# Optimization experiments

Hardware: AMD Instinct MI355X
Metric: run time of the kernel (lower is better)

## Reference

```python
import jax, jax.numpy as jnp
import numpy as np

NUM_EMBEDDINGS = 1024
EMBEDDING_DIM = 256
BETA = 0.25


def setup_inputs() -> dict:
    key = jax.random.key(0)
    k1, k2 = jax.random.split(key)
    inputs = jax.random.normal(k1, (32, EMBEDDING_DIM, 64, 64), dtype=jnp.float32)
    # codebook init: uniform(-1/K, 1/K), matching nn.Embedding init in the module
    embedding = jax.random.uniform(
        k2, (NUM_EMBEDDINGS, EMBEDDING_DIM), dtype=jnp.float32,
        minval=-1.0 / NUM_EMBEDDINGS, maxval=1.0 / NUM_EMBEDDINGS)
    return {"inputs": inputs, "embedding": embedding, "beta": BETA}


def reference(inputs, embedding, beta):
    # inputs: [B, D, H, W] -> [B, H, W, D]
    x = jnp.transpose(inputs, (0, 2, 3, 1))
    in_shape = x.shape
    flat = x.reshape(-1, embedding.shape[1])  # [N, D]
    dist = (jnp.sum(flat * flat, axis=1, keepdims=True)
            + jnp.sum(embedding * embedding, axis=1)
            - 2.0 * flat @ embedding.T)
    codebook_indices = jnp.argmin(dist, axis=1)  # [N]
    quantized = embedding[codebook_indices].reshape(in_shape)  # [B,H,W,D]
    sg = jax.lax.stop_gradient
    e_latent_loss = beta * jnp.mean((sg(quantized) - x) ** 2)
    q_latent_loss = jnp.mean((quantized - sg(x)) ** 2)
    loss = e_latent_loss + q_latent_loss
    # straight-through estimator
    quantized_st = x + sg(quantized - x)
    return loss, jnp.transpose(quantized_st, (0, 3, 1, 2))
```

## Files before the change

kernel.cpp:

```cpp
#include <hip/hip_runtime.h>
#include <hip/hip_bf16.h>


#define DIN 256
#define NCODES 1024

typedef __attribute__((ext_vector_type(8))) short short8;
typedef __attribute__((ext_vector_type(4))) float float4v;
typedef __attribute__((ext_vector_type(2))) float float2v;
typedef __attribute__((ext_vector_type(4))) unsigned short ushort4v;

static __device__ __forceinline__ unsigned short f2bf(float f) {
  unsigned int u = __float_as_uint(f);
  unsigned int r = (u + 0x7fffu + ((u >> 16) & 1u)) >> 16;
  return (unsigned short)r;
}

__global__ void vq_prep(const float* __restrict__ e,
                        unsigned short* __restrict__ e_bf2,
                        float* __restrict__ norms) {
  int wave = threadIdx.x >> 6, lane = threadIdx.x & 63;
  int k = blockIdx.x * 4 + wave;
  float4v v = ((const float4v*)(e + k * DIN))[lane];
  float ss = v[0]*v[0] + v[1]*v[1] + v[2]*v[2] + v[3]*v[3];
  ushort4v pk;
  pk[0] = f2bf(v[0]); pk[1] = f2bf(v[1]); pk[2] = f2bf(v[2]); pk[3] = f2bf(v[3]);
  int cc = lane >> 1, sub = lane & 1;
  *(ushort4v*)(e_bf2 + (cc * NCODES + k) * 8 + sub * 4) = pk;
  #pragma unroll
  for (int m = 1; m < 64; m <<= 1) ss += __shfl_xor(ss, m, 64);
  if (lane == 0) norms[k] = ss;
}

__global__ void __launch_bounds__(256, 4)
vq_main(const float* __restrict__ xin, const float* __restrict__ e_fp,
        const unsigned short* __restrict__ e_bf2, const float* __restrict__ norms,
        float* __restrict__ out, float* __restrict__ loss_acc) {
  __shared__ char smem[34080];
  unsigned short* es = (unsigned short*)smem;
  float* qs  = (float*)smem;
  float* vs  = (float*)(smem + 32768);
  int*   is_ = (int*)  (smem + 33280);
  int*   fi  = (int*)  (smem + 33792);
  float* rs  = (float*)(smem + 34048);

  const int tid  = threadIdx.x;
  const int wave = tid >> 6, lane = tid & 63;
  const int m16  = lane & 15, quad = lane >> 4;
  const int wr   = wave >> 1, wc = wave & 1;
  const int b    = blockIdx.x >> 6, h = blockIdx.x & 63;
  const int base = b * 1048576 + h * 64;

  short8 areg[16];
  #pragma unroll
  for (int i = 0; i < 2; ++i) {
    int r = wr * 32 + i * 16 + m16;
    #pragma unroll
    for (int kk = 0; kk < 8; ++kk) {
      int cc = kk * 4 + quad;
      short8 pk;
      #pragma unroll
      for (int ii = 0; ii < 8; ++ii)
        pk[ii] = (short)f2bf(xin[base + (cc * 8 + ii) * 4096 + r]);
      areg[i * 8 + kk] = pk;
    }
  }

  float bestv[2][4];
  int   besti[2][4];
  float4v acc[2][2];
  #pragma unroll
  for (int i = 0; i < 2; ++i) {
    #pragma unroll
    for (int r = 0; r < 4; ++r) { bestv[i][r] = INFINITY; besti[i][r] = 0; }
    #pragma unroll
    for (int j = 0; j < 2; ++j) acc[i][j] = (float4v)(0.0f);
  }

  for (int ct = 0; ct < 16; ++ct) {
    int c0 = ct * 64;
    #pragma unroll
    for (int q = 0; q < 8; ++q) {
      int cc8 = wave * 8 + q;
      const unsigned short* gsrc = e_bf2 + (cc8 * NCODES + c0) * 8 + lane * 8;
      unsigned short* ldst = es + cc8 * 512;
      __builtin_amdgcn_global_load_lds(
          (const __attribute__((address_space(1))) void*)gsrc,
          (__attribute__((address_space(3))) void*)ldst, 16, 0, 0);
    }
    __syncthreads();
    #pragma unroll
    for (int kk = 0; kk < 8; ++kk) {
      int cc = kk * 4 + quad;
      short8 b0 = *(short8*)(es + (cc * 64 + wc * 32 + m16) * 8);
      short8 b1 = *(short8*)(es + (cc * 64 + wc * 32 + 16 + m16) * 8);
      acc[0][0] = __builtin_amdgcn_mfma_f32_16x16x32_bf16(areg[kk],     b0, acc[0][0], 0, 0, 0);
      acc[0][1] = __builtin_amdgcn_mfma_f32_16x16x32_bf16(areg[kk],     b1, acc[0][1], 0, 0, 0);
      acc[1][0] = __builtin_amdgcn_mfma_f32_16x16x32_bf16(areg[8 + kk], b0, acc[1][0], 0, 0, 0);
      acc[1][1] = __builtin_amdgcn_mfma_f32_16x16x32_bf16(areg[8 + kk], b1, acc[1][1], 0, 0, 0);
    }
    #pragma unroll
    for (int j = 0; j < 2; ++j) {
      int col = c0 + wc * 32 + j * 16 + m16;
      float nj = norms[col];
      #pragma unroll
      for (int i = 0; i < 2; ++i) {
        #pragma unroll
        for (int r = 0; r < 4; ++r) {
          float s = nj - 2.0f * acc[i][j][r];
          if (s < bestv[i][r]) { bestv[i][r] = s; besti[i][r] = col; }
        }
        acc[i][j] = (float4v)(0.0f);
      }
    }
    __syncthreads();
  }

  #pragma unroll
  for (int msk = 1; msk <= 8; msk <<= 1) {
    #pragma unroll
    for (int i = 0; i < 2; ++i)
      #pragma unroll
      for (int r = 0; r < 4; ++r) {
        float ov = __shfl_xor(bestv[i][r], msk, 64);
        int   oi = __shfl_xor(besti[i][r], msk, 64);
        if (ov < bestv[i][r] || (ov == bestv[i][r] && oi < besti[i][r])) {
          bestv[i][r] = ov; besti[i][r] = oi;
        }
      }
  }
  if (m16 == 0) {
    #pragma unroll
    for (int i = 0; i < 2; ++i)
      #pragma unroll
      for (int r = 0; r < 4; ++r) {
        int rl = wr * 32 + i * 16 + quad * 4 + r;
        vs [rl * 2 + wc] = bestv[i][r];
        is_[rl * 2 + wc] = besti[i][r];
      }
  }
  __syncthreads();
  if (tid < 64) {
    float v0 = vs[tid * 2], v1 = vs[tid * 2 + 1];
    int   i0 = is_[tid * 2], i1 = is_[tid * 2 + 1];
    fi[tid] = (v1 < v0 || (v1 == v0 && i1 < i0)) ? i1 : i0;
  }
  __syncthreads();

  float lsum = 0.0f;
  const int wq = tid & 31, dL0 = tid >> 5;
  for (int h2 = 0; h2 < 4; ++h2) {
    #pragma unroll
    for (int j = 0; j < 4; ++j) {
      int f = j * 256 + tid;
      int w2 = f >> 4, cc = f & 15;
      int idx = fi[w2];
      float4v qv = *(const float4v*)(e_fp + idx * DIN + h2 * 64 + cc * 4);
      #pragma unroll
      for (int ii = 0; ii < 4; ++ii)
        qs[(cc * 4 + ii) * 66 + w2] = qv[ii];
    }
    __syncthreads();
    #pragma unroll
    for (int dd = 0; dd < 8; ++dd) {
      int dL = dd * 8 + dL0;
      int g = base + (h2 * 64 + dL) * 4096 + wq * 2;
      float2v q  = *(float2v*)(qs + dL * 66 + wq * 2);
      float2v xv = *(const float2v*)(xin + g);
      out[1 + g] = q[0];
      out[2 + g] = q[1];
      float d0 = q[0] - xv[0], d1 = q[1] - xv[1];
      lsum += d0 * d0 + d1 * d1;
    }
    __syncthreads();
  }

  #pragma unroll
  for (int msk = 1; msk < 64; msk <<= 1) lsum += __shfl_xor(lsum, msk, 64);
  if (lane == 0) rs[wave] = lsum;
  __syncthreads();
  if (tid == 0) atomicAdd(loss_acc, rs[0] + rs[1] + rs[2] + rs[3]);
}

__global__ void vq_fin(const float* __restrict__ loss_acc,
                       const float* __restrict__ beta,
                       float* __restrict__ out) {
  out[0] = (1.0f + beta[0]) * loss_acc[0] / 33554432.0f;
}

extern "C" void kernel_launch(void* const* d_in, const int* in_sizes, int n_in,
                              void* d_out, int out_size, void* d_ws, size_t ws_size,
                              hipStream_t stream) {
  const float* xin  = (const float*)d_in[0];
  const float* emb  = (const float*)d_in[1];
  const float* beta = (const float*)d_in[2];
  float* out = (float*)d_out;
  float* loss_acc = (float*)d_ws;
  float* norms = (float*)((char*)d_ws + 4096);
  unsigned short* e_bf2 = (unsigned short*)((char*)d_ws + 8192);

  hipMemsetAsync(d_ws, 0, 4, stream);
  vq_prep<<<256, 256, 0, stream>>>(emb, e_bf2, norms);
  vq_main<<<2048, 256, 0, stream>>>(xin, emb, e_bf2, norms, out, loss_acc);
  vq_fin<<<1, 1, 0, stream>>>(loss_acc, beta, out);
}
```

Measured before the change: 365.3 us.

## Give each wave a full 64-pixel row and read codebook straight from global

```diff
diff --git a/kernel.cpp b/kernel.cpp
--- a/kernel.cpp
+++ b/kernel.cpp
@@ -32,94 +32,74 @@
   if (lane == 0) norms[k] = ss;
 }
 
-__global__ void __launch_bounds__(256, 4)
+__global__ void __launch_bounds__(256, 2)
 vq_main(const float* __restrict__ xin, const float* __restrict__ e_fp,
         const unsigned short* __restrict__ e_bf2, const float* __restrict__ norms,
         float* __restrict__ out, float* __restrict__ loss_acc) {
-  __shared__ char smem[34080];
-  unsigned short* es = (unsigned short*)smem;
-  float* qs  = (float*)smem;
-  float* vs  = (float*)(smem + 32768);
-  int*   is_ = (int*)  (smem + 33280);
-  int*   fi  = (int*)  (smem + 33792);
-  float* rs  = (float*)(smem + 34048);
+  __shared__ float qs[4][64 * 66];
+  __shared__ int   fi[4][64];
 
   const int tid  = threadIdx.x;
   const int wave = tid >> 6, lane = tid & 63;
   const int m16  = lane & 15, quad = lane >> 4;
-  const int wr   = wave >> 1, wc = wave & 1;
-  const int b    = blockIdx.x >> 6, h = blockIdx.x & 63;
+  const int line = blockIdx.x * 4 + wave;
+  const int b    = line >> 6, h = line & 63;
   const int base = b * 1048576 + h * 64;
 
-  short8 areg[16];
+  short8 areg[32];
   #pragma unroll
-  for (int i = 0; i < 2; ++i) {
-    int r = wr * 32 + i * 16 + m16;
+  for (int i = 0; i < 4; ++i) {
+    int r = i * 16 + m16;
     #pragma unroll
     for (int kk = 0; kk < 8; ++kk) {
-      int cc = kk * 4 + quad;
+      int d0 = (kk * 4 + quad) * 8;
       short8 pk;
       #pragma unroll
       for (int ii = 0; ii < 8; ++ii)
-        pk[ii] = (short)f2bf(xin[base + (cc * 8 + ii) * 4096 + r]);
+        pk[ii] = (short)f2bf(xin[base + (d0 + ii) * 4096 + r]);
       areg[i * 8 + kk] = pk;
     }
   }
 
-  float bestv[2][4];
-  int   besti[2][4];
-  float4v acc[2][2];
+  float bestv[4][4];
+  int   besti[4][4];
+  float4v acc[4];
   #pragma unroll
-  for (int i = 0; i < 2; ++i) {
+  for (int i = 0; i < 4; ++i) {
     #pragma unroll
     for (int r = 0; r < 4; ++r) { bestv[i][r] = INFINITY; besti[i][r] = 0; }
-    #pragma unroll
-    for (int j = 0; j < 2; ++j) acc[i][j] = (float4v)(0.0f);
+    acc[i] = (float4v)(0.0f);
   }
 
-  for (int ct = 0; ct < 16; ++ct) {
-    int c0 = ct * 64;
+  for (int cs = 0; cs < 64; ++cs) {
+    int c0 = cs * 16;
+    short8 bfr[8];
     #pragma unroll
-    for (int q = 0; q < 8; ++q) {
-      int cc8 = wave * 8 + q;
-      const unsigned short* gsrc = e_bf2 + (cc8 * NCODES + c0) * 8 + lane * 8;
-      unsigned short* ldst = es + cc8 * 512;
-      __builtin_amdgcn_global_load_lds(
-          (const __attribute__((address_space(1))) void*)gsrc,
-          (__attribute__((address_space(3))) void*)ldst, 16, 0, 0);
-    }
-    __syncthreads();
+    for (int kk = 0; kk < 8; ++kk)
+      bfr[kk] = *(const short8*)(e_bf2 + ((kk * 4 + quad) * NCODES + c0 + m16) * 8);
+    float nj = norms[c0 + m16];
     #pragma unroll
     for (int kk = 0; kk < 8; ++kk) {
-      int cc = kk * 4 + quad;
-      short8 b0 = *(short8*)(es + (cc * 64 + wc * 32 + m16) * 8);
-      short8 b1 = *(short8*)(es + (cc * 64 + wc * 32 + 16 + m16) * 8);
-      acc[0][0] = __builtin_amdgcn_mfma_f32_16x16x32_bf16(areg[kk],     b0, acc[0][0], 0, 0, 0);
-      acc[0][1] = __builtin_amdgcn_mfma_f32_16x16x32_bf16(areg[kk],     b1, acc[0][1], 0, 0, 0);
-      acc[1][0] = __builtin_amdgcn_mfma_f32_16x16x32_bf16(areg[8 + kk], b0, acc[1][0], 0, 0, 0);
-      acc[1][1] = __builtin_amdgcn_mfma_f32_16x16x32_bf16(areg[8 + kk], b1, acc[1][1], 0, 0, 0);
+      #pragma unroll
+      for (int i = 0; i < 4; ++i)
+        acc[i] = __builtin_amdgcn_mfma_f32_16x16x32_bf16(areg[i * 8 + kk], bfr[kk], acc[i], 0, 0, 0);
     }
+    int col = c0 + m16;
     #pragma unroll
-    for (int j = 0; j < 2; ++j) {
-      int col = c0 + wc * 32 + j * 16 + m16;
-      float nj = norms[col];
+    for (int i = 0; i < 4; ++i) {
       #pragma unroll
-      for (int i = 0; i < 2; ++i) {
-        #pragma unroll
-        for (int r = 0; r < 4; ++r) {
-          float s = nj - 2.0f * acc[i][j][r];
-          if (s < bestv[i][r]) { bestv[i][r] = s; besti[i][r] = col; }
-        }
-        acc[i][j] = (float4v)(0.0f);
+      for (int r = 0; r < 4; ++r) {
+        float s = nj - 2.0f * acc[i][r];
+        if (s < bestv[i][r]) { bestv[i][r] = s; besti[i][r] = col; }
       }
+      acc[i] = (float4v)(0.0f);
     }
-    __syncthreads();
   }
 
   #pragma unroll
   for (int msk = 1; msk <= 8; msk <<= 1) {
     #pragma unroll
-    for (int i = 0; i < 2; ++i)
+    for (int i = 0; i < 4; ++i)
       #pragma unroll
       for (int r = 0; r < 4; ++r) {
         float ov = __shfl_xor(bestv[i][r], msk, 64);
@@ -131,55 +111,45 @@
   }
   if (m16 == 0) {
     #pragma unroll
-    for (int i = 0; i < 2; ++i)
+    for (int i = 0; i < 4; ++i)
       #pragma unroll
-      for (int r = 0; r < 4; ++r) {
-        int rl = wr * 32 + i * 16 + quad * 4 + r;
-        vs [rl * 2 + wc] = bestv[i][r];
-        is_[rl * 2 + wc] = besti[i][r];
-      }
+      for (int r = 0; r < 4; ++r)
+        fi[wave][i * 16 + quad * 4 + r] = besti[i][r];
   }
-  __syncthreads();
-  if (tid < 64) {
-    float v0 = vs[tid * 2], v1 = vs[tid * 2 + 1];
-    int   i0 = is_[tid * 2], i1 = is_[tid * 2 + 1];
-    fi[tid] = (v1 < v0 || (v1 == v0 && i1 < i0)) ? i1 : i0;
-  }
-  __syncthreads();
+  __asm__ volatile("s_waitcnt lgkmcnt(0)" ::: "memory");
 
+  float* qsw = qs[wave];
+  const int* fiw = fi[wave];
   float lsum = 0.0f;
-  const int wq = tid & 31, dL0 = tid >> 5;
+  const int wq = lane & 31, dh = lane >> 5;
   for (int h2 = 0; h2 < 4; ++h2) {
     #pragma unroll
-    for (int j = 0; j < 4; ++j) {
-      int f = j * 256 + tid;
-      int w2 = f >> 4, cc = f & 15;
-      int idx = fi[w2];
-      float4v qv = *(const float4v*)(e_fp + idx * DIN + h2 * 64 + cc * 4);
+    for (int jj = 0; jj < 16; ++jj) {
+      int w2 = jj * 4 + quad;
+      int idx = fiw[w2];
+      float4v qv = *(const float4v*)(e_fp + idx * DIN + h2 * 64 + m16 * 4);
       #pragma unroll
       for (int ii = 0; ii < 4; ++ii)
-        qs[(cc * 4 + ii) * 66 + w2] = qv[ii];
+        qsw[(m16 * 4 + ii) * 66 + w2] = qv[ii];
     }
-    __syncthreads();
+    __asm__ volatile("s_waitcnt lgkmcnt(0)" ::: "memory");
     #pragma unroll
-    for (int dd = 0; dd < 8; ++dd) {
-      int dL = dd * 8 + dL0;
+    for (int dd = 0; dd < 32; ++dd) {
+      int dL = dd * 2 + dh;
       int g = base + (h2 * 64 + dL) * 4096 + wq * 2;
-      float2v q  = *(float2v*)(qs + dL * 66 + wq * 2);
+      float2v q  = *(float2v*)(qsw + dL * 66 + wq * 2);
       float2v xv = *(const float2v*)(xin + g);
       out[1 + g] = q[0];
       out[2 + g] = q[1];
       float d0 = q[0] - xv[0], d1 = q[1] - xv[1];
       lsum += d0 * d0 + d1 * d1;
     }
-    __syncthreads();
+    __asm__ volatile("s_waitcnt lgkmcnt(0)" ::: "memory");
   }
 
   #pragma unroll
   for (int msk = 1; msk < 64; msk <<= 1) lsum += __shfl_xor(lsum, msk, 64);
-  if (lane == 0) rs[wave] = lsum;
-  __syncthreads();
-  if (tid == 0) atomicAdd(loss_acc, rs[0] + rs[1] + rs[2] + rs[3]);
+  if (lane == 0) atomicAdd(loss_acc, lsum);
 }
 
 __global__ void vq_fin(const float* __restrict__ loss_acc,
@@ -201,6 +171,6 @@
 
   hipMemsetAsync(d_ws, 0, 4, stream);
   vq_prep<<<256, 256, 0, stream>>>(emb, e_bf2, norms);
-  vq_main<<<2048, 256, 0, stream>>>(xin, emb, e_bf2, norms, out, loss_acc);
+  vq_main<<<512, 256, 0, stream>>>(xin, emb, e_bf2, norms, out, loss_acc);
   vq_fin<<<1, 1, 0, stream>>>(loss_acc, beta, out);
 }
```

Measured after the change: 401.7 us. 1.1x slower.
